# Performance work log

Hardware: AMD Instinct MI355X
Metric: run time of the kernel (lower is better)

The kernel has to match this reference:

```python
import jax, jax.numpy as jnp
import numpy as np

N_LABELS = 16
LABEL_DIM = 128
BN_EPS = 1e-5


def setup_inputs() -> dict:
    key = jax.random.key(0)
    k1, k2 = jax.random.split(key, 2)
    B, T, D = 8, 512, 768
    return {
        "features": jax.random.normal(k1, (B, T, D), dtype=jnp.float32),
        "mask": jnp.ones((B, T), dtype=bool),
        "bn_gamma": jnp.ones((D,), dtype=jnp.float32),
        "bn_beta": jnp.zeros((D,), dtype=jnp.float32),
        "ff_w": jax.random.normal(k2, (LABEL_DIM * N_LABELS * 2, D), dtype=jnp.float32) * 0.02,
        "ff_b": jnp.zeros((LABEL_DIM * N_LABELS * 2,), dtype=jnp.float32),
        "label_bias": jnp.zeros((N_LABELS,), dtype=jnp.float32),
    }


def reference(features, mask, bn_gamma, bn_beta, ff_w, ff_b, label_bias):
    B, T, D = features.shape
    m = mask.astype(features.dtype)[..., None]  # [B,T,1]
    denom = jnp.maximum(m.sum(), 1.0)
    # FlatBatchNorm (training mode): stats over masked tokens, zeros elsewhere
    mean = (features * m).sum(axis=(0, 1)) / denom
    var = (((features - mean) ** 2) * m).sum(axis=(0, 1)) / denom
    normed = (features - mean) * jax.lax.rsqrt(var + BN_EPS) * bn_gamma + bn_beta
    feats = normed * m  # res[mask]=flat, zeros elsewhere
    # FFN + relu -> [B,T,n_labels,label_dim,2]
    h = jax.nn.relu(jnp.einsum('btd,od->bto', feats, ff_w) + ff_b)
    h = h.reshape(B, T, N_LABELS, LABEL_DIM, 2)
    start_f = h[..., 0]  # [B,T,L,D]
    end_f = h[..., 1]
    # biaffine span scores: [B, L, T_start, T_end]
    scores = jnp.einsum('bsld,beld->blse', start_f, end_f) + label_bias[None, :, None, None]
    triu = jnp.triu(jnp.ones((T, T), dtype=bool))
    spans_mask = triu[None, None] & mask[:, None, :, None] & mask[:, None, None, :]  # [B,L,T,T] via broadcast
    spans_mask = jnp.broadcast_to(spans_mask, scores.shape)
    return scores, spans_mask
```

## Files before the change

### kernel.cpp

```cpp
#include <hip/hip_runtime.h>

#define B_    8
#define T_    512
#define D_    768
#define L_    16
#define DL_   128
#define NO_   4096
#define M_    4096
#define BN_EPS 1e-5f

typedef __attribute__((ext_vector_type(8))) short short8;
typedef __attribute__((ext_vector_type(4))) float f32x4;
typedef __attribute__((ext_vector_type(2))) float f32x2;

__device__ inline unsigned short f2bf(float x) {
    unsigned int u = __float_as_uint(x);
    unsigned int r = (u + 0x7fffu + ((u >> 16) & 1u)) >> 16;
    return (unsigned short)r;
}

__device__ __forceinline__ void gload_lds16(const unsigned short* g, unsigned short* l) {
    __builtin_amdgcn_global_load_lds(
        (const __attribute__((address_space(1))) unsigned int*)g,
        (__attribute__((address_space(3))) unsigned int*)l, 16, 0, 0);
}

__global__ void k_stats(const float* __restrict__ f, const int* __restrict__ mask,
                        float* __restrict__ stats) {
    int tid = threadIdx.x;
    int t0  = blockIdx.x * 16;
    float s0 = 0.f, s1 = 0.f, s2 = 0.f, q0 = 0.f, q1 = 0.f, q2 = 0.f;
    for (int tt = 0; tt < 16; ++tt) {
        int t = t0 + tt;
        float m = mask[t] ? 1.f : 0.f;
        const float* row = f + (size_t)t * D_;
        float x0 = row[tid];
        float x1 = row[tid + 256];
        float x2 = row[tid + 512];
        s0 += x0 * m; q0 += x0 * x0 * m;
        s1 += x1 * m; q1 += x1 * x1 * m;
        s2 += x2 * m; q2 += x2 * x2 * m;
    }
    atomicAdd(&stats[tid      ], s0);
    atomicAdd(&stats[tid + 256], s1);
    atomicAdd(&stats[tid + 512], s2);
    atomicAdd(&stats[768 + tid      ], q0);
    atomicAdd(&stats[768 + tid + 256], q1);
    atomicAdd(&stats[768 + tid + 512], q2);
    if (tid == 0) {
        int c = 0;
        for (int tt = 0; tt < 16; ++tt) c += (mask[t0 + tt] ? 1 : 0);
        atomicAdd(&stats[1536], (float)c);
    }
}

__global__ void k_finalize(const float* __restrict__ gamma, const float* __restrict__ beta,
                           float* __restrict__ stats) {
    int d = threadIdx.x;
    float denom = fmaxf(stats[1536], 1.f);
    float mean  = stats[d] / denom;
    float var   = fmaxf(stats[768 + d] / denom - mean * mean, 0.f);
    float sc    = gamma[d] * rsqrtf(var + BN_EPS);
    stats[2048 + d] = sc;
    stats[2816 + d] = beta[d] - mean * sc;
}

__global__ void k_normcast(const float4* __restrict__ f4, const float4* __restrict__ w4,
                           const int* __restrict__ mask, const float* __restrict__ stats,
                           unsigned short* __restrict__ featp, unsigned short* __restrict__ wp) {
    int i = blockIdx.x * 256 + threadIdx.x;
    if (i < M_ * D_ / 4) {
        int d4 = i % (D_ / 4);
        int t  = i / (D_ / 4);
        float m = mask[t] ? 1.f : 0.f;
        float4 v = f4[i];
        int d = d4 * 4;
        float r0 = (v.x * stats[2048 + d + 0] + stats[2816 + d + 0]) * m;
        float r1 = (v.y * stats[2048 + d + 1] + stats[2816 + d + 1]) * m;
        float r2 = (v.z * stats[2048 + d + 2] + stats[2816 + d + 2]) * m;
        float r3 = (v.w * stats[2048 + d + 3] + stats[2816 + d + 3]) * m;
        ushort4 o;
        o.x = f2bf(r0); o.y = f2bf(r1); o.z = f2bf(r2); o.w = f2bf(r3);
        ((ushort4*)featp)[i] = o;
    } else {
        int j = i - M_ * D_ / 4;
        float4 v = w4[j];
        ushort4 o;
        o.x = f2bf(v.x); o.y = f2bf(v.y); o.z = f2bf(v.z); o.w = f2bf(v.w);
        ((ushort4*)wp)[j] = o;
    }
}

__launch_bounds__(512, 2)
__global__ void k_ffn(const unsigned short* __restrict__ A, const unsigned short* __restrict__ W,
                      const float* __restrict__ bias,
                      unsigned short* __restrict__ startp, unsigned short* __restrict__ endp) {
    __shared__ alignas(16) unsigned short LA[4][8192];
    __shared__ alignas(16) unsigned short LB[4][8192];
    int h   = blockIdx.x;
    int xcd = h & 7, q = h >> 3;
    int bm  = xcd * 4 + (q >> 5);
    int bn  = q & 31;
    int tid  = threadIdx.x;
    int wave = tid >> 6, lane = tid & 63;
    int wm = wave >> 2, wn = wave & 3;
    int lr = lane & 15, quad = lane >> 4;
    int srow = lane >> 3;
    int sg   = (lane & 7) ^ srow;
    const unsigned short* asrc[2];
    const unsigned short* bsrc[2];
#pragma unroll
    for (int p = 0; p < 2; ++p) {
        int c = wave * 2 + p;
        asrc[p] = A + (size_t)(bm * 128 + c * 8 + srow) * D_ + sg * 8;
        bsrc[p] = W + (size_t)(bn * 128 + c * 8 + srow) * D_ + sg * 8;
    }
    int aoff[4][2], boff[2][2];
#pragma unroll
    for (int i = 0; i < 4; ++i)
#pragma unroll
        for (int kk = 0; kk < 2; ++kk) {
            int row = wm * 64 + i * 16 + lr;
            aoff[i][kk] = row * 64 + ((kk * 4 + quad) ^ (row & 7)) * 8;
        }
#pragma unroll
    for (int j = 0; j < 2; ++j)
#pragma unroll
        for (int kk = 0; kk < 2; ++kk) {
            int row = wn * 32 + j * 16 + lr;
            boff[j][kk] = row * 64 + ((kk * 4 + quad) ^ (row & 7)) * 8;
        }
    f32x4 acc[4][2] = {};
#pragma unroll
    for (int t = 0; t < 2; ++t) {
#pragma unroll
        for (int p = 0; p < 2; ++p) {
            int c = wave * 2 + p;
            gload_lds16(asrc[p] + t * 64, &LA[t][c * 512]);
            gload_lds16(bsrc[p] + t * 64, &LB[t][c * 512]);
        }
    }
#pragma unroll
    for (int t = 0; t < 12; ++t) {
        if (t == 11) asm volatile("s_waitcnt vmcnt(0)\ns_barrier" ::: "memory");
        else         asm volatile("s_waitcnt vmcnt(4)\ns_barrier" ::: "memory");
        const unsigned short* la = LA[t & 3];
        const unsigned short* lb = LB[t & 3];
        short8 af[4][2], bf[2][2];
#pragma unroll
        for (int i = 0; i < 4; ++i)
#pragma unroll
            for (int kk = 0; kk < 2; ++kk)
                af[i][kk] = *(const short8*)&la[aoff[i][kk]];
#pragma unroll
        for (int j = 0; j < 2; ++j)
#pragma unroll
            for (int kk = 0; kk < 2; ++kk)
                bf[j][kk] = *(const short8*)&lb[boff[j][kk]];
        if (t < 10) {
            int ss = (t + 2) & 3;
            int ko = (t + 2) * 64;
#pragma unroll
            for (int p = 0; p < 2; ++p) {
                int c = wave * 2 + p;
                gload_lds16(asrc[p] + ko, &LA[ss][c * 512]);
                gload_lds16(bsrc[p] + ko, &LB[ss][c * 512]);
            }
        }
        __builtin_amdgcn_s_setprio(1);
#pragma unroll
        for (int kk = 0; kk < 2; ++kk)
#pragma unroll
            for (int i = 0; i < 4; ++i)
#pragma unroll
                for (int j = 0; j < 2; ++j)
                    acc[i][j] = __builtin_amdgcn_mfma_f32_16x16x32_bf16(af[i][kk], bf[j][kk], acc[i][j], 0, 0, 0);
        __builtin_amdgcn_s_setprio(0);
    }
#pragma unroll
    for (int i = 0; i < 4; ++i) {
#pragma unroll
        for (int j = 0; j < 2; ++j) {
            int col  = bn * 128 + wn * 32 + j * 16 + lr;
            int l    = col >> 8;
            int dd   = (col >> 1) & 127;
            int cbit = col & 1;
            unsigned short* dst = cbit ? endp : startp;
            float bv = bias[col];
#pragma unroll
            for (int r = 0; r < 4; ++r) {
                int row = bm * 128 + wm * 64 + i * 16 + quad * 4 + r;
                float v = acc[i][j][r] + bv;
                v = fmaxf(v, 0.f);
                int bb = row >> 9, tt = row & 511;
                dst[(((size_t)(bb * 16 + l) * 512 + tt) << 7) + dd] = f2bf(v);
            }
        }
    }
}

__launch_bounds__(256)
__global__ void k_biaffine(const unsigned short* __restrict__ startp,
                           const unsigned short* __restrict__ endp,
                           const int* __restrict__ mask,
                           const float* __restrict__ lbias,
                           float* __restrict__ out_scores, float* __restrict__ out_mask) {
    __shared__ alignas(16) float smemf[64 * 132];
    unsigned short* As = (unsigned short*)smemf;
    unsigned short* Bs = As + 128 * 64;
    float* Cs = smemf;
    int hgrid = blockIdx.x;
    int xcd = hgrid & 7, q = hgrid >> 3;
    int bl  = xcd * 16 + (q >> 4);
    int inner = q & 15;
    int bm = inner & 3, bn = inner >> 2;
    int b  = bl >> 4;
    int tid = threadIdx.x;
    const unsigned short* A  = startp + (size_t)bl * 512 * 128;
    const unsigned short* Bp = endp   + (size_t)bl * 512 * 128;
    int wave = tid >> 6, lane = tid & 63;
    int wm = wave >> 1, wn = wave & 1;
    int lr = lane & 15, quad = lane >> 4;
    f32x4 acc[4][4] = {};
    int srow = lane >> 3;
    for (int half = 0; half < 2; ++half) {
#pragma unroll
        for (int p = 0; p < 4; ++p) {
            int c   = wave * 4 + p;
            int row = c * 8 + srow;
            int gl  = (lane & 7) ^ (row & 7);
            gload_lds16(A  + (size_t)(bm * 128 + row) * DL_ + half * 64 + gl * 8, &As[c * 512]);
            gload_lds16(Bp + (size_t)(bn * 128 + row) * DL_ + half * 64 + gl * 8, &Bs[c * 512]);
        }
        __syncthreads();
#pragma unroll
        for (int kk = 0; kk < 2; ++kk) {
            short8 a[4], bb[4];
#pragma unroll
            for (int i = 0; i < 4; ++i) {
                int row = wm * 64 + i * 16 + lr;
                int gp  = (kk * 4 + quad) ^ (row & 7);
                a[i] = *(const short8*)&As[row * 64 + gp * 8];
            }
#pragma unroll
            for (int j = 0; j < 4; ++j) {
                int row = wn * 64 + j * 16 + lr;
                int gp  = (kk * 4 + quad) ^ (row & 7);
                bb[j] = *(const short8*)&Bs[row * 64 + gp * 8];
            }
#pragma unroll
            for (int i = 0; i < 4; ++i)
#pragma unroll
                for (int j = 0; j < 4; ++j)
                    acc[i][j] = __builtin_amdgcn_mfma_f32_16x16x32_bf16(a[i], bb[j], acc[i][j], 0, 0, 0);
        }
        __syncthreads();
    }
    float lb = lbias[bl & 15];
    float* obase = out_scores + (size_t)bl * 512 * 512;
    float* mbase = out_mask   + (size_t)bl * 512 * 512;
    int e0 = bn * 128 + lane * 2;
    float me0 = mask[b * 512 + e0    ] ? 1.f : 0.f;
    float me1 = mask[b * 512 + e0 + 1] ? 1.f : 0.f;
    for (int hh = 0; hh < 2; ++hh) {
        if (wm == hh) {
#pragma unroll
            for (int i = 0; i < 4; ++i)
#pragma unroll
                for (int j = 0; j < 4; ++j)
#pragma unroll
                    for (int r = 0; r < 4; ++r)
                        Cs[(i * 16 + quad * 4 + r) * 132 + wn * 64 + j * 16 + lr] = acc[i][j][r];
        }
        __syncthreads();
#pragma unroll
        for (int rr = 0; rr < 16; ++rr) {
            int rloc = wave * 16 + rr;
            int s = bm * 128 + hh * 64 + rloc;
            f32x2 v = *(const f32x2*)&Cs[rloc * 132 + lane * 2];
            v.x += lb; v.y += lb;
            float ms = mask[b * 512 + s] ? 1.f : 0.f;
            f32x2 mk;
            mk.x = (s <= e0    ) ? ms * me0 : 0.f;
            mk.y = (s <= e0 + 1) ? ms * me1 : 0.f;
            size_t off = (size_t)s * 512 + e0;
            __builtin_nontemporal_store(v,  (f32x2*)&obase[off]);
            __builtin_nontemporal_store(mk, (f32x2*)&mbase[off]);
        }
        __syncthreads();
    }
}

extern "C" void kernel_launch(void* const* d_in, const int* in_sizes, int n_in,
                              void* d_out, int out_size, void* d_ws, size_t ws_size,
                              hipStream_t stream) {
    const float* features = (const float*)d_in[0];
    const int*   mask     = (const int*)d_in[1];
    const float* gamma    = (const float*)d_in[2];
    const float* beta     = (const float*)d_in[3];
    const float* ffw      = (const float*)d_in[4];
    const float* ffb      = (const float*)d_in[5];
    const float* lbias    = (const float*)d_in[6];

    float* out_scores = (float*)d_out;
    float* out_mask   = out_scores + (size_t)B_ * L_ * T_ * T_;

    char* ws = (char*)d_ws;
    float*          stats  = (float*)ws;
    unsigned short* feats  = (unsigned short*)(ws + 16384);
    unsigned short* wbf    = (unsigned short*)(ws + 16384 + 6291456);
    unsigned short* startp = (unsigned short*)(ws + 12599296);
    unsigned short* endp   = (unsigned short*)(ws + 29376512);

    hipMemsetAsync(ws, 0, 16384, stream);
    k_stats<<<256, 256, 0, stream>>>(features, mask, stats);
    k_finalize<<<1, 768, 0, stream>>>(gamma, beta, stats);
    k_normcast<<<6144, 256, 0, stream>>>((const float4*)features, (const float4*)ffw,
                                         mask, stats, feats, wbf);
    k_ffn<<<1024, 512, 0, stream>>>(feats, wbf, ffb, startp, endp);
    k_biaffine<<<2048, 256, 0, stream>>>(startp, endp, mask, lbias, out_scores, out_mask);
}
```

Baseline: 358.5 us.

## Fold BN finalize into normcast and stage FFN epilogue through LDS for coalesced stores

Removes the single-block finalize kernel by recomputing per-channel scale and shift inside the normalize/cast kernel, which saves one launch at the cost of redundant per-thread arithmetic. The FFN epilogue now writes bias+ReLU bf16 results into shared memory, de-interleaving start/end columns, then emits 16-byte coalesced stores to the start and end buffers. The old epilogue used scattered 2-byte stores. This adds two barriers and reuses the A tile buffer as staging space.

```diff
diff --git a/kernel.cpp b/kernel.cpp
--- a/kernel.cpp
+++ b/kernel.cpp
@@ -54,19 +54,9 @@
     }
 }
 
-__global__ void k_finalize(const float* __restrict__ gamma, const float* __restrict__ beta,
-                           float* __restrict__ stats) {
-    int d = threadIdx.x;
-    float denom = fmaxf(stats[1536], 1.f);
-    float mean  = stats[d] / denom;
-    float var   = fmaxf(stats[768 + d] / denom - mean * mean, 0.f);
-    float sc    = gamma[d] * rsqrtf(var + BN_EPS);
-    stats[2048 + d] = sc;
-    stats[2816 + d] = beta[d] - mean * sc;
-}
-
 __global__ void k_normcast(const float4* __restrict__ f4, const float4* __restrict__ w4,
                            const int* __restrict__ mask, const float* __restrict__ stats,
+                           const float* __restrict__ gamma, const float* __restrict__ beta,
                            unsigned short* __restrict__ featp, unsigned short* __restrict__ wp) {
     int i = blockIdx.x * 256 + threadIdx.x;
     if (i < M_ * D_ / 4) {
@@ -75,10 +65,20 @@
         float m = mask[t] ? 1.f : 0.f;
         float4 v = f4[i];
         int d = d4 * 4;
-        float r0 = (v.x * stats[2048 + d + 0] + stats[2816 + d + 0]) * m;
-        float r1 = (v.y * stats[2048 + d + 1] + stats[2816 + d + 1]) * m;
-        float r2 = (v.z * stats[2048 + d + 2] + stats[2816 + d + 2]) * m;
-        float r3 = (v.w * stats[2048 + d + 3] + stats[2816 + d + 3]) * m;
+        float denom = fmaxf(stats[1536], 1.f);
+        float sc[4], sh[4];
+#pragma unroll
+        for (int c = 0; c < 4; ++c) {
+            float mean = stats[d + c] / denom;
+            float var  = fmaxf(stats[768 + d + c] / denom - mean * mean, 0.f);
+            float s    = gamma[d + c] * rsqrtf(var + BN_EPS);
+            sc[c] = s;
+            sh[c] = beta[d + c] - mean * s;
+        }
+        float r0 = (v.x * sc[0] + sh[0]) * m;
+        float r1 = (v.y * sc[1] + sh[1]) * m;
+        float r2 = (v.z * sc[2] + sh[2]) * m;
+        float r3 = (v.w * sc[3] + sh[3]) * m;
         ushort4 o;
         o.x = f2bf(r0); o.y = f2bf(r1); o.z = f2bf(r2); o.w = f2bf(r3);
         ((ushort4*)featp)[i] = o;
@@ -177,25 +177,40 @@
                     acc[i][j] = __builtin_amdgcn_mfma_f32_16x16x32_bf16(af[i][kk], bf[j][kk], acc[i][j], 0, 0, 0);
         __builtin_amdgcn_s_setprio(0);
     }
+    __syncthreads();
+    unsigned short* C16 = &LA[0][0];
 #pragma unroll
     for (int i = 0; i < 4; ++i) {
 #pragma unroll
         for (int j = 0; j < 2; ++j) {
-            int col  = bn * 128 + wn * 32 + j * 16 + lr;
-            int l    = col >> 8;
-            int dd   = (col >> 1) & 127;
-            int cbit = col & 1;
-            unsigned short* dst = cbit ? endp : startp;
-            float bv = bias[col];
+            int col_local = wn * 32 + j * 16 + lr;
+            float bv = bias[bn * 128 + col_local];
+            int a   = col_local & 1;
+            int ddp = col_local >> 1;
 #pragma unroll
             for (int r = 0; r < 4; ++r) {
-                int row = bm * 128 + wm * 64 + i * 16 + quad * 4 + r;
-                float v = acc[i][j][r] + bv;
-                v = fmaxf(v, 0.f);
-                int bb = row >> 9, tt = row & 511;
-                dst[(((size_t)(bb * 16 + l) * 512 + tt) << 7) + dd] = f2bf(v);
+                int row = wm * 64 + i * 16 + quad * 4 + r;
+                float v = fmaxf(acc[i][j][r] + bv, 0.f);
+                C16[row * 136 + a * 64 + ddp] = f2bf(v);
             }
         }
+    }
+    __syncthreads();
+    int bb     = bm >> 2;
+    int l      = bn >> 1;
+    int ddbase = (bn & 1) * 64;
+#pragma unroll
+    for (int it = 0; it < 4; ++it) {
+        int flat  = it * 512 + tid;
+        int piece = flat & 7;
+        int run   = flat >> 3;
+        int a     = run & 1;
+        int row   = run >> 1;
+        int tt    = (bm & 3) * 128 + row;
+        uint4 v = *(const uint4*)&C16[row * 136 + a * 64 + piece * 8];
+        unsigned short* dst = a ? endp : startp;
+        size_t off = ((size_t)(bb * 16 + l) * 512 + tt) * 128 + ddbase + piece * 8;
+        *(uint4*)&dst[off] = v;
     }
 }
 
@@ -314,9 +329,8 @@
 
     hipMemsetAsync(ws, 0, 16384, stream);
     k_stats<<<256, 256, 0, stream>>>(features, mask, stats);
-    k_finalize<<<1, 768, 0, stream>>>(gamma, beta, stats);
     k_normcast<<<6144, 256, 0, stream>>>((const float4*)features, (const float4*)ffw,
-                                         mask, stats, feats, wbf);
+                                         mask, stats, gamma, beta, feats, wbf);
     k_ffn<<<1024, 512, 0, stream>>>(feats, wbf, ffb, startp, endp);
     k_biaffine<<<2048, 256, 0, stream>>>(startp, endp, mask, lbias, out_scores, out_mask);
 }
```

Result: faster. 351.3 us (-2.0%).
